# Optimization experiments

Measured on AMD Instinct MI355X. Metric: run time of the kernel, lower is better.

Reference implementation:

```python
import jax, jax.numpy as jnp
import numpy as np

N_NODES = 100000
N_EDGES = 1600000
IN_CH, HID_CH, OUT_CH, NCLASS = 128, 256, 256, 40


def gcn_conv(x, edge_index, edge_weight, W, b):
    """PyG GCNConv: h = D^{-1/2} (A + I) D^{-1/2} (x @ W) + b, weighted edges."""
    n = x.shape[0]
    row, col = edge_index[0], edge_index[1]
    loop = jnp.arange(n)
    row = jnp.concatenate([row, loop])
    col = jnp.concatenate([col, loop])
    ew = jnp.concatenate([edge_weight, jnp.ones((n,), x.dtype)])  # self-loop weight 1
    deg = jax.ops.segment_sum(ew, col, num_segments=n)
    dinv = jnp.where(deg > 0, jax.lax.rsqrt(deg), 0.0)
    norm = dinv[row] * ew * dinv[col]            # [E+N]
    h = x @ W                                    # transform before propagate (as PyG)
    msg = h[row] * norm[:, None]                 # gather + scale, [E+N, F]
    out = jax.ops.segment_sum(msg, col, num_segments=n)  # scatter-add
    return out + b


def setup_inputs() -> dict:
    key = jax.random.key(0)
    ks = jax.random.split(key, 9)
    x = jax.random.normal(ks[0], (N_NODES, IN_CH), dtype=jnp.float32)
    edge_index = jax.random.randint(ks[1], (2, N_EDGES), 0, N_NODES, dtype=jnp.int64)
    edge_attr = jax.random.uniform(ks[2], (N_EDGES,), dtype=jnp.float32)
    s1 = 1.0 / np.sqrt(IN_CH)
    s2 = 1.0 / np.sqrt(HID_CH)
    s3 = 1.0 / np.sqrt(OUT_CH)
    W1 = jax.random.uniform(ks[3], (IN_CH, HID_CH), jnp.float32, -s1, s1)
    b1 = jnp.zeros((HID_CH,), jnp.float32)
    W2 = jax.random.uniform(ks[4], (HID_CH, OUT_CH), jnp.float32, -s2, s2)
    b2 = jnp.zeros((OUT_CH,), jnp.float32)
    fcW = jax.random.uniform(ks[5], (OUT_CH, NCLASS), jnp.float32, -s3, s3)
    fcb = jax.random.uniform(ks[6], (NCLASS,), jnp.float32, -s3, s3)
    return {"x": x, "edge_index": edge_index, "edge_attr": edge_attr,
            "W1": W1, "b1": b1, "W2": W2, "b2": b2, "fcW": fcW, "fcb": fcb}


def reference(x, edge_index, edge_attr, W1, b1, W2, b2, fcW, fcb):
    # eval mode: dropout is identity
    h = jax.nn.relu(gcn_conv(x, edge_index, edge_attr, W1, b1))
    h = jax.nn.relu(gcn_conv(h, edge_index, edge_attr, W2, b2))
    return h @ fcW + fcb
```

## Files before the change

kernel.cpp:

```cpp
#include <hip/hip_runtime.h>

#define NODES 100000
#define EDGES 1600000

typedef __attribute__((ext_vector_type(4))) float floatx4;
typedef _Float16 h16;
typedef __attribute__((ext_vector_type(4))) _Float16 h16x4;
typedef __attribute__((ext_vector_type(8))) _Float16 h16x8;
typedef __attribute__((ext_vector_type(8))) _Float16 half8;

#define WSCALE 64.0f
#define WINV   (1.0f / 64.0f)

__device__ inline void load_lds16(void* lds, const void* g) {
    __builtin_amdgcn_global_load_lds((const __attribute__((address_space(1))) void*)g,
                                     (__attribute__((address_space(3))) void*)lds, 16, 0, 0);
}

__device__ inline float meta_w(unsigned m) {
    return (float)__builtin_bit_cast(h16, (unsigned short)(m & 0x7FFFu));
}

__global__ __launch_bounds__(256) void k_init(unsigned long long* __restrict__ packed, int n) {
    int i = blockIdx.x * 256 + threadIdx.x;
    if (i < n) packed[i] = 0ull;
}

__device__ inline void w_split(const float* W, h16* Wh, h16* Wl, int idx, int K) {
    int k = idx >> 8, nn = idx & 255;
    float v = W[idx] * WSCALE;
    h16 h = (h16)v;
    h16 l = (h16)(v - (float)h);
    Wh[nn * K + k] = h;
    Wl[nn * K + k] = l;
}

__global__ __launch_bounds__(256) void k_hist(unsigned long long* __restrict__ packed,
                                              unsigned short* __restrict__ rank,
                                              const int* __restrict__ col,
                                              const float* __restrict__ ew, int e,
                                              const float* __restrict__ W1, h16* __restrict__ W1h, h16* __restrict__ W1l,
                                              const float* __restrict__ W2, h16* __restrict__ W2h, h16* __restrict__ W2l,
                                              const float* __restrict__ x, h16* __restrict__ x16, int n) {
    int b = blockIdx.x;
    if (b < 6250) {
        int i = b * 256 + threadIdx.x;
        if (i < e) {
            int c = col[i];
            unsigned long long v = (1ull << 40) |
                (unsigned long long)__float2uint_rn(ew[i] * 1048576.0f);
            unsigned long long old = atomicAdd(&packed[c], v);
            rank[i] = (unsigned short)(old >> 40);
        }
    } else if (b < 6378) {
        w_split(W1, W1h, W1l, (b - 6250) * 256 + threadIdx.x, 128);
    } else if (b < 6634) {
        w_split(W2, W2h, W2l, (b - 6378) * 256 + threadIdx.x, 256);
    } else {
        int i = (b - 6634) * 256 + threadIdx.x;
        if (i < n * 32) {
            float4 v = reinterpret_cast<const float4*>(x)[i];
            h16x4 h;
            h.x = (h16)v.x; h.y = (h16)v.y; h.z = (h16)v.z; h.w = (h16)v.w;
            reinterpret_cast<h16x4*>(x16)[i] = h;
        }
    }
}

__global__ __launch_bounds__(256) void k_scan1(const unsigned long long* __restrict__ packed,
                                               int* __restrict__ rowptr,
                                               int* __restrict__ partials,
                                               float* __restrict__ dinv, int n) {
    __shared__ int wtot[4];
    const int tid = threadIdx.x, lane = tid & 63, wid = tid >> 6;
    int i = blockIdx.x * 256 + tid;
    int v = 0;
    if (i < n) {
        unsigned long long p = packed[i];
        v = (int)(p >> 40);
        float deg = 1.0f + (float)(p & 0xFFFFFFFFFFull) * (1.0f / 1048576.0f);
        dinv[i] = rsqrtf(deg);
    }
    int incl = v;
#pragma unroll
    for (int off = 1; off < 64; off <<= 1) {
        int t = __shfl_up(incl, off, 64);
        if (lane >= off) incl += t;
    }
    if (lane == 63) wtot[wid] = incl;
    __syncthreads();
    int woff = 0;
    for (int k = 0; k < wid; ++k) woff += wtot[k];
    if (i < n) rowptr[i] = woff + incl - v;
    if (tid == 255) partials[blockIdx.x] = woff + incl;
}

__global__ __launch_bounds__(512) void k_scan2(int* __restrict__ partials, int nb) {
    __shared__ int wtot[8];
    const int tid = threadIdx.x, lane = tid & 63, wid = tid >> 6;
    int v = (tid < nb) ? partials[tid] : 0;
    int incl = v;
#pragma unroll
    for (int off = 1; off < 64; off <<= 1) {
        int t = __shfl_up(incl, off, 64);
        if (lane >= off) incl += t;
    }
    if (lane == 63) wtot[wid] = incl;
    __syncthreads();
    int woff = 0;
    for (int k = 0; k < wid; ++k) woff += wtot[k];
    if (tid < nb) partials[tid] = woff + incl - v;
}

__global__ __launch_bounds__(256) void k_scan3(int* __restrict__ rowptr,
                                               const int* __restrict__ partials, int n) {
    int i = blockIdx.x * 256 + threadIdx.x;
    if (i < n) rowptr[i] += partials[blockIdx.x];
    if (blockIdx.x == 0 && threadIdx.x == 0) rowptr[n] = EDGES;
}

__global__ __launch_bounds__(256) void k_build(const int* __restrict__ rowptr,
                                               const unsigned short* __restrict__ rank,
                                               unsigned* __restrict__ meta,
                                               const int* __restrict__ row, const int* __restrict__ col,
                                               const float* __restrict__ ew,
                                               const float* __restrict__ dinv, int e) {
    int i = blockIdx.x * 256 + threadIdx.x;
    if (i >= e) return;
    int r = row[i], c = col[i];
    float w = dinv[r] * ew[i] * dinv[c];
    unsigned short wb = __builtin_bit_cast(unsigned short, (h16)w);
    meta[rowptr[c] + rank[i]] = ((unsigned)r << 15) | wb;
}

__global__ __launch_bounds__(256) void k_gather_x(h16* __restrict__ Xa,
                                                  const h16* __restrict__ x16,
                                                  const float* __restrict__ dinv,
                                                  const int* __restrict__ rowptr,
                                                  const unsigned* __restrict__ meta, int n) {
    int node = (blockIdx.x << 2) + (threadIdx.x >> 6);
    if (node >= n) return;
    const int lane = threadIdx.x & 63;
    const int half = lane >> 5;
    const int cb = (lane & 31) << 2;
    float a0[4] = {}, a1[4] = {};
    int p = rowptr[node];
    const int end = rowptr[node + 1];
    for (; p + 3 < end; p += 4) {
        unsigned m0 = meta[p + half], m1 = meta[p + half + 2];
        h16x4 h0 = *(const h16x4*)(x16 + (size_t)(m0 >> 15) * 128 + cb);
        h16x4 h1 = *(const h16x4*)(x16 + (size_t)(m1 >> 15) * 128 + cb);
        float w0 = meta_w(m0), w1 = meta_w(m1);
#pragma unroll
        for (int j = 0; j < 4; ++j) {
            a0[j] = fmaf((float)h0[j], w0, a0[j]);
            a1[j] = fmaf((float)h1[j], w1, a1[j]);
        }
    }
    for (; p + 1 < end; p += 2) {
        unsigned m0 = meta[p + half];
        h16x4 h0 = *(const h16x4*)(x16 + (size_t)(m0 >> 15) * 128 + cb);
        float w0 = meta_w(m0);
#pragma unroll
        for (int j = 0; j < 4; ++j) a0[j] = fmaf((float)h0[j], w0, a0[j]);
    }
    if (half == 0 && p < end) {
        unsigned m0 = meta[p];
        h16x4 h0 = *(const h16x4*)(x16 + (size_t)(m0 >> 15) * 128 + cb);
        float w0 = meta_w(m0);
#pragma unroll
        for (int j = 0; j < 4; ++j) a1[j] = fmaf((float)h0[j], w0, a1[j]);
    }
#pragma unroll
    for (int j = 0; j < 4; ++j) a0[j] += a1[j];
#pragma unroll
    for (int j = 0; j < 4; ++j) a0[j] += __shfl(a0[j], lane + 32);
    if (half == 0) {
        float s = dinv[node]; s = s * s;
        h16x4 sv = *(const h16x4*)(x16 + (size_t)node * 128 + cb);
        h16x4 o;
#pragma unroll
        for (int j = 0; j < 4; ++j) o[j] = (h16)fmaf((float)sv[j], s, a0[j]);
        *(h16x4*)(Xa + (size_t)node * 128 + cb) = o;
    }
}

__global__ __launch_bounds__(256) void k_gather_y(h16* __restrict__ Y,
                                                  const h16* __restrict__ P1,
                                                  const float* __restrict__ dinv,
                                                  const int* __restrict__ rowptr,
                                                  const unsigned* __restrict__ meta, int n) {
    int node = (blockIdx.x << 2) + (threadIdx.x >> 6);
    if (node >= n) return;
    const int lane = threadIdx.x & 63;
    const int half = lane >> 5;
    const int cb = (lane & 31) << 3;
    float a0[8] = {}, a1[8] = {};
    int p = rowptr[node];
    const int end = rowptr[node + 1];
    for (; p + 3 < end; p += 4) {
        unsigned m0 = meta[p + half], m1 = meta[p + half + 2];
        h16x8 h0 = *(const h16x8*)(P1 + (size_t)(m0 >> 15) * 256 + cb);
        h16x8 h1 = *(const h16x8*)(P1 + (size_t)(m1 >> 15) * 256 + cb);
        float w0 = meta_w(m0), w1 = meta_w(m1);
#pragma unroll
        for (int j = 0; j < 8; ++j) {
            a0[j] = fmaf((float)h0[j], w0, a0[j]);
            a1[j] = fmaf((float)h1[j], w1, a1[j]);
        }
    }
    for (; p + 1 < end; p += 2) {
        unsigned m0 = meta[p + half];
        h16x8 h0 = *(const h16x8*)(P1 + (size_t)(m0 >> 15) * 256 + cb);
        float w0 = meta_w(m0);
#pragma unroll
        for (int j = 0; j < 8; ++j) a0[j] = fmaf((float)h0[j], w0, a0[j]);
    }
    if (half == 0 && p < end) {
        unsigned m0 = meta[p];
        h16x8 h0 = *(const h16x8*)(P1 + (size_t)(m0 >> 15) * 256 + cb);
        float w0 = meta_w(m0);
#pragma unroll
        for (int j = 0; j < 8; ++j) a1[j] = fmaf((float)h0[j], w0, a1[j]);
    }
#pragma unroll
    for (int j = 0; j < 8; ++j) a0[j] += a1[j];
#pragma unroll
    for (int j = 0; j < 8; ++j) a0[j] += __shfl(a0[j], lane + 32);
    if (half == 0) {
        float s = dinv[node]; s = s * s;
        h16x8 sv = *(const h16x8*)(P1 + (size_t)node * 256 + cb);
        h16x8 o;
#pragma unroll
        for (int j = 0; j < 8; ++j) o[j] = (h16)fmaf((float)sv[j], s, a0[j]);
        *(h16x8*)(Y + (size_t)node * 256 + cb) = o;
    }
}

__global__ __launch_bounds__(256) void k_gemm(const h16* __restrict__ Ag,
                                              const h16* __restrict__ Bhg,
                                              const h16* __restrict__ Blg,
                                              h16* __restrict__ Out,
                                              const float* __restrict__ bias,
                                              int M, int K) {
    __shared__ __attribute__((aligned(16))) char ldsA[8192];
    __shared__ __attribute__((aligned(16))) char ldsBh[8192];
    __shared__ __attribute__((aligned(16))) char ldsBl[8192];
    const int tid = threadIdx.x;
    const int lane = tid & 63, wid = tid >> 6;
    const int quad = lane >> 4, l16 = lane & 15;
    const int rowBase = blockIdx.x * 128;
    const int colBase = blockIdx.y * 128;
    const int wm = (wid & 1) * 64, wn = (wid >> 1) * 64;

    floatx4 acc[4][4] = {};

    const int c0 = wid * 64 + lane;
    const int c1 = c0 + 256;
    const int r0 = ((c0 >> 6) << 4) + (c0 & 15), q0 = (c0 >> 4) & 3;
    const int r1 = ((c1 >> 6) << 4) + (c1 & 15), q1 = (c1 >> 4) & 3;
    const size_t aoff0 = (size_t)(rowBase + r0) * K + q0 * 8;
    const size_t aoff1 = (size_t)(rowBase + r1) * K + q1 * 8;
    const size_t boff0 = (size_t)(colBase + r0) * K + q0 * 8;
    const size_t boff1 = (size_t)(colBase + r1) * K + q1 * 8;
    const int lo0 = (wid * 64) * 16;
    const int lo1 = (256 + wid * 64) * 16;

    for (int k0 = 0; k0 < K; k0 += 32) {
        load_lds16(ldsA + lo0, Ag + aoff0 + k0);
        load_lds16(ldsA + lo1, Ag + aoff1 + k0);
        load_lds16(ldsBh + lo0, Bhg + boff0 + k0);
        load_lds16(ldsBh + lo1, Bhg + boff1 + k0);
        load_lds16(ldsBl + lo0, Blg + boff0 + k0);
        load_lds16(ldsBl + lo1, Blg + boff1 + k0);
        __syncthreads();

        const half8* vA  = (const half8*)ldsA;
        const half8* vBh = (const half8*)ldsBh;
        const half8* vBl = (const half8*)ldsBl;
        half8 af[4], bfh[4], bfl[4];
#pragma unroll
        for (int mi = 0; mi < 4; ++mi)
            af[mi] = vA[((wm >> 4) + mi) * 64 + quad * 16 + l16];
#pragma unroll
        for (int ni = 0; ni < 4; ++ni) {
            int idx = ((wn >> 4) + ni) * 64 + quad * 16 + l16;
            bfh[ni] = vBh[idx];
            bfl[ni] = vBl[idx];
        }
#pragma unroll
        for (int mi = 0; mi < 4; ++mi)
#pragma unroll
            for (int ni = 0; ni < 4; ++ni) {
                acc[mi][ni] = __builtin_amdgcn_mfma_f32_16x16x32_f16(af[mi], bfh[ni], acc[mi][ni], 0, 0, 0);
                acc[mi][ni] = __builtin_amdgcn_mfma_f32_16x16x32_f16(af[mi], bfl[ni], acc[mi][ni], 0, 0, 0);
            }
        __syncthreads();
    }

#pragma unroll
    for (int mi = 0; mi < 4; ++mi) {
#pragma unroll
        for (int r = 0; r < 4; ++r) {
            int grow = rowBase + wm + mi * 16 + quad * 4 + r;
            if (grow < M) {
#pragma unroll
                for (int ni = 0; ni < 4; ++ni) {
                    int gcol = colBase + wn + ni * 16 + l16;
                    float v = fmaxf(acc[mi][ni][r] * WINV + bias[gcol], 0.f);
                    Out[(size_t)grow * 256 + gcol] = (h16)v;
                }
            }
        }
    }
}

__global__ __launch_bounds__(256) void k_fc(float* __restrict__ out, const h16* __restrict__ X,
                                            const float* __restrict__ W, const float* __restrict__ bias,
                                            int M) {
    __shared__ float Ws[256 * 40];
    __shared__ float Xs[32][69];
    const int tid = threadIdx.x;
#pragma unroll
    for (int t = 0; t < 10; ++t) {
        int idx = (t * 256 + tid) * 4;
        *reinterpret_cast<float4*>(&Ws[idx]) = *reinterpret_cast<const float4*>(W + idx);
    }
    const int rowBase = blockIdx.x * 64;
    const int r  = tid >> 2;
    const int cg = (tid & 3) * 10;
    const int kq = (tid & 3) << 3;
    float acc[10] = {};

    for (int k0 = 0; k0 < 256; k0 += 32) {
        int rr = rowBase + r;
        h16x8 v = {};
        if (rr < M) v = *reinterpret_cast<const h16x8*>(X + (size_t)rr * 256 + k0 + kq);
#pragma unroll
        for (int j = 0; j < 8; ++j) Xs[kq + j][r] = (float)v[j];
        __syncthreads();
#pragma unroll
        for (int kk = 0; kk < 32; ++kk) {
            float xv = Xs[kk][r];
#pragma unroll
            for (int j = 0; j < 10; ++j)
                acc[j] = fmaf(xv, Ws[(k0 + kk) * 40 + cg + j], acc[j]);
        }
        __syncthreads();
    }

    int orow = rowBase + r;
    if (orow < M) {
#pragma unroll
        for (int j = 0; j < 10; ++j)
            out[(size_t)orow * 40 + cg + j] = acc[j] + bias[cg + j];
    }
}

extern "C" void kernel_launch(void* const* d_in, const int* in_sizes, int n_in,
                              void* d_out, int out_size, void* d_ws, size_t ws_size,
                              hipStream_t stream) {
    const float* x   = (const float*)d_in[0];
    const int*   ei  = (const int*)d_in[1];
    const float* ea  = (const float*)d_in[2];
    const float* W1  = (const float*)d_in[3];
    const float* b1  = (const float*)d_in[4];
    const float* W2  = (const float*)d_in[5];
    const float* b2  = (const float*)d_in[6];
    const float* fcW = (const float*)d_in[7];
    const float* fcb = (const float*)d_in[8];
    float* out = (float*)d_out;

    const int n = NODES, e = EDGES;
    const int* row = ei;
    const int* col = ei + e;

    char* ws = (char*)d_ws;
    char*  Areg   = ws;
    char*  Breg   = ws + 102400000u;
    float* dinv   = (float*)(ws + 204800000u);
    unsigned long long* packed = (unsigned long long*)(ws + 205200000u);
    int*   rowptr = (int*)  (ws + 206000000u);
    unsigned* meta = (unsigned*)(ws + 206400016u);
    h16*   W1h    = (h16*)  (ws + 212800016u);
    h16*   W1l    = (h16*)  (ws + 212865552u);
    h16*   W2h    = (h16*)  (ws + 212931088u);
    h16*   W2l    = (h16*)  (ws + 213062160u);

    int* partials = (int*)Areg;
    h16* Xa16 = (h16*)Areg;
    h16* x16  = (h16*)(Areg + 25600000u);
    h16* Yh   = (h16*)Areg;
    unsigned short* rank = (unsigned short*)Breg;
    h16* P1   = (h16*)Breg;
    h16* P2h  = (h16*)(Breg + 51200000u);

    const int nb = (n + 255) / 256;
    const int eb = e / 256;

    k_init<<<nb, 256, 0, stream>>>(packed, n);
    k_hist<<<19134, 256, 0, stream>>>(packed, rank, col, ea, e,
                                      W1, W1h, W1l, W2, W2h, W2l, x, x16, n);
    k_scan1<<<nb, 256, 0, stream>>>(packed, rowptr, partials, dinv, n);
    k_scan2<<<1, 512, 0, stream>>>(partials, nb);
    k_scan3<<<nb, 256, 0, stream>>>(rowptr, partials, n);
    k_build<<<eb, 256, 0, stream>>>(rowptr, rank, meta, row, col, ea, dinv, e);

    dim3 gg((n + 127) / 128, 2);

    k_gather_x<<<(n + 3) / 4, 256, 0, stream>>>(Xa16, x16, dinv, rowptr, meta, n);
    k_gemm<<<gg, 256, 0, stream>>>(Xa16, W1h, W1l, P1, b1, n, 128);

    k_gather_y<<<(n + 3) / 4, 256, 0, stream>>>(Yh, P1, dinv, rowptr, meta, n);
    k_gemm<<<gg, 256, 0, stream>>>(Yh, W2h, W2l, P2h, b2, n, 256);

    k_fc<<<(n + 63) / 64, 256, 0, stream>>>(out, P2h, fcW, fcb, n);
}
```

Baseline: 612.2 us.

## Use MFMA for final FC, fold scan2 into scan3, add nontemporal stores

```diff
diff --git a/kernel.cpp b/kernel.cpp
--- a/kernel.cpp
+++ b/kernel.cpp
@@ -95,28 +95,21 @@
     if (tid == 255) partials[blockIdx.x] = woff + incl;
 }
 
-__global__ __launch_bounds__(512) void k_scan2(int* __restrict__ partials, int nb) {
-    __shared__ int wtot[8];
-    const int tid = threadIdx.x, lane = tid & 63, wid = tid >> 6;
-    int v = (tid < nb) ? partials[tid] : 0;
-    int incl = v;
-#pragma unroll
-    for (int off = 1; off < 64; off <<= 1) {
-        int t = __shfl_up(incl, off, 64);
-        if (lane >= off) incl += t;
-    }
-    if (lane == 63) wtot[wid] = incl;
-    __syncthreads();
-    int woff = 0;
-    for (int k = 0; k < wid; ++k) woff += wtot[k];
-    if (tid < nb) partials[tid] = woff + incl - v;
-}
-
 __global__ __launch_bounds__(256) void k_scan3(int* __restrict__ rowptr,
                                                const int* __restrict__ partials, int n) {
-    int i = blockIdx.x * 256 + threadIdx.x;
-    if (i < n) rowptr[i] += partials[blockIdx.x];
-    if (blockIdx.x == 0 && threadIdx.x == 0) rowptr[n] = EDGES;
+    __shared__ int wsum[4];
+    const int tid = threadIdx.x, lane = tid & 63, wid = tid >> 6;
+    const int b = blockIdx.x;
+    int v = 0;
+    for (int t = tid; t < b; t += 256) v += partials[t];
+#pragma unroll
+    for (int off = 32; off > 0; off >>= 1) v += __shfl_down(v, off, 64);
+    if (lane == 0) wsum[wid] = v;
+    __syncthreads();
+    int base = wsum[0] + wsum[1] + wsum[2] + wsum[3];
+    int i = b * 256 + tid;
+    if (i < n) rowptr[i] += base;
+    if (b == 0 && tid == 0) rowptr[n] = EDGES;
 }
 
 __global__ __launch_bounds__(256) void k_build(const int* __restrict__ rowptr,
@@ -181,7 +174,7 @@
         h16x4 o;
 #pragma unroll
         for (int j = 0; j < 4; ++j) o[j] = (h16)fmaf((float)sv[j], s, a0[j]);
-        *(h16x4*)(Xa + (size_t)node * 128 + cb) = o;
+        __builtin_nontemporal_store(o, (h16x4*)(Xa + (size_t)node * 128 + cb));
     }
 }
 
@@ -233,10 +226,11 @@
         h16x8 o;
 #pragma unroll
         for (int j = 0; j < 8; ++j) o[j] = (h16)fmaf((float)sv[j], s, a0[j]);
-        *(h16x8*)(Y + (size_t)node * 256 + cb) = o;
-    }
-}
-
+        __builtin_nontemporal_store(o, (h16x8*)(Y + (size_t)node * 256 + cb));
+    }
+}
+
+template<bool NT>
 __global__ __launch_bounds__(256) void k_gemm(const h16* __restrict__ Ag,
                                               const h16* __restrict__ Bhg,
                                               const h16* __restrict__ Blg,
@@ -308,7 +302,8 @@
                 for (int ni = 0; ni < 4; ++ni) {
                     int gcol = colBase + wn + ni * 16 + l16;
                     float v = fmaxf(acc[mi][ni][r] * WINV + bias[gcol], 0.f);
-                    Out[(size_t)grow * 256 + gcol] = (h16)v;
+                    if (NT) __builtin_nontemporal_store((h16)v, Out + (size_t)grow * 256 + gcol);
+                    else Out[(size_t)grow * 256 + gcol] = (h16)v;
                 }
             }
         }
@@ -318,43 +313,66 @@
 __global__ __launch_bounds__(256) void k_fc(float* __restrict__ out, const h16* __restrict__ X,
                                             const float* __restrict__ W, const float* __restrict__ bias,
                                             int M) {
-    __shared__ float Ws[256 * 40];
-    __shared__ float Xs[32][69];
+    __shared__ __attribute__((aligned(16))) char ldsB[24576];
+    __shared__ __attribute__((aligned(16))) char ldsA[8192];
     const int tid = threadIdx.x;
-#pragma unroll
-    for (int t = 0; t < 10; ++t) {
-        int idx = (t * 256 + tid) * 4;
-        *reinterpret_cast<float4*>(&Ws[idx]) = *reinterpret_cast<const float4*>(W + idx);
-    }
-    const int rowBase = blockIdx.x * 64;
-    const int r  = tid >> 2;
-    const int cg = (tid & 3) * 10;
-    const int kq = (tid & 3) << 3;
-    float acc[10] = {};
-
-    for (int k0 = 0; k0 < 256; k0 += 32) {
-        int rr = rowBase + r;
+    const int lane = tid & 63, wid = tid >> 6;
+    const int quad = lane >> 4, l16 = lane & 15;
+    const int rowBase = blockIdx.x * 128;
+
+    for (int c = tid; c < 1536; c += 256) {
+        int idx = c & 63, s = (c >> 6) & 7, t = c >> 9;
+        int q = idx >> 4, nn = t * 16 + (idx & 15);
+        int kb = s * 32 + q * 8;
         h16x8 v = {};
-        if (rr < M) v = *reinterpret_cast<const h16x8*>(X + (size_t)rr * 256 + k0 + kq);
-#pragma unroll
-        for (int j = 0; j < 8; ++j) Xs[kq + j][r] = (float)v[j];
+        if (nn < 40) {
+#pragma unroll
+            for (int j = 0; j < 8; ++j) v[j] = (h16)W[(kb + j) * 40 + nn];
+        }
+        *reinterpret_cast<h16x8*>(ldsB + c * 16) = v;
+    }
+
+    floatx4 acc[2][3] = {};
+    const int c0 = wid * 64 + lane;
+    const int c1 = c0 + 256;
+    const int r0 = ((c0 >> 6) << 4) + (c0 & 15), q0 = (c0 >> 4) & 3;
+    const int r1 = ((c1 >> 6) << 4) + (c1 & 15), q1 = (c1 >> 4) & 3;
+
+    for (int s = 0; s < 8; ++s) {
+        int k0 = s * 32;
+        load_lds16(ldsA + c0 * 16, X + (size_t)(rowBase + r0) * 256 + k0 + q0 * 8);
+        load_lds16(ldsA + c1 * 16, X + (size_t)(rowBase + r1) * 256 + k0 + q1 * 8);
         __syncthreads();
-#pragma unroll
-        for (int kk = 0; kk < 32; ++kk) {
-            float xv = Xs[kk][r];
-#pragma unroll
-            for (int j = 0; j < 10; ++j)
-                acc[j] = fmaf(xv, Ws[(k0 + kk) * 40 + cg + j], acc[j]);
+        const half8* vA = (const half8*)ldsA;
+        const half8* vB = (const half8*)ldsB;
+        half8 af[2];
+#pragma unroll
+        for (int mi = 0; mi < 2; ++mi)
+            af[mi] = vA[(wid * 2 + mi) * 64 + quad * 16 + l16];
+#pragma unroll
+        for (int t = 0; t < 3; ++t) {
+            half8 bf = vB[(t * 8 + s) * 64 + quad * 16 + l16];
+#pragma unroll
+            for (int mi = 0; mi < 2; ++mi)
+                acc[mi][t] = __builtin_amdgcn_mfma_f32_16x16x32_f16(af[mi], bf, acc[mi][t], 0, 0, 0);
         }
         __syncthreads();
     }
 
-    int orow = rowBase + r;
-    if (orow < M) {
-#pragma unroll
-        for (int j = 0; j < 10; ++j)
-            out[(size_t)orow * 40 + cg + j] = acc[j] + bias[cg + j];
-    }
+#pragma unroll
+    for (int mi = 0; mi < 2; ++mi)
+#pragma unroll
+        for (int r = 0; r < 4; ++r) {
+            int grow = rowBase + wid * 32 + mi * 16 + quad * 4 + r;
+            if (grow < M) {
+#pragma unroll
+                for (int t = 0; t < 3; ++t) {
+                    int gcol = t * 16 + l16;
+                    if (gcol < 40)
+                        out[(size_t)grow * 40 + gcol] = acc[mi][t][r] + bias[gcol];
+                }
+            }
+        }
 }
 
 extern "C" void kernel_launch(void* const* d_in, const int* in_sizes, int n_in,
@@ -402,17 +420,16 @@
     k_hist<<<19134, 256, 0, stream>>>(packed, rank, col, ea, e,
                                       W1, W1h, W1l, W2, W2h, W2l, x, x16, n);
     k_scan1<<<nb, 256, 0, stream>>>(packed, rowptr, partials, dinv, n);
-    k_scan2<<<1, 512, 0, stream>>>(partials, nb);
     k_scan3<<<nb, 256, 0, stream>>>(rowptr, partials, n);
     k_build<<<eb, 256, 0, stream>>>(rowptr, rank, meta, row, col, ea, dinv, e);
 
     dim3 gg((n + 127) / 128, 2);
 
     k_gather_x<<<(n + 3) / 4, 256, 0, stream>>>(Xa16, x16, dinv, rowptr, meta, n);
-    k_gemm<<<gg, 256, 0, stream>>>(Xa16, W1h, W1l, P1, b1, n, 128);
+    k_gemm<false><<<gg, 256, 0, stream>>>(Xa16, W1h, W1l, P1, b1, n, 128);
 
     k_gather_y<<<(n + 3) / 4, 256, 0, stream>>>(Yh, P1, dinv, rowptr, meta, n);
-    k_gemm<<<gg, 256, 0, stream>>>(Yh, W2h, W2l, P2h, b2, n, 256);
-
-    k_fc<<<(n + 63) / 64, 256, 0, stream>>>(out, P2h, fcW, fcb, n);
-}
+    k_gemm<true><<<gg, 256, 0, stream>>>(Yh, W2h, W2l, P2h, b2, n, 256);
+
+    k_fc<<<(n + 127) / 128, 256, 0, stream>>>(out, P2h, fcW, fcb, n);
+}
```

After: 556.0 us. -9.2%, faster.
